# Optimization experiments

Measured on AMD Instinct MI355X. Metric: run time of the kernel, lower is better.

The kernel has to match this reference:

```python
import jax, jax.numpy as jnp
import numpy as np

EPS = 1e-6
NEG_SLOPE = 0.2


def _basis(J):
    # J: [B,N,E,3] -> R: [B,N,E,3(k: U,V,J rows),3(xyz comp)]
    nJ = J / (jnp.linalg.norm(J, axis=-1, keepdims=True) + EPS)
    sub = nJ[..., :2]
    u_z = -(sub[..., 0] ** 2 + sub[..., 1] ** 2) / (nJ[..., 2] + EPS)
    U = jnp.concatenate([sub, u_z[..., None]], axis=-1)
    U = U / (jnp.linalg.norm(U, axis=-1, keepdims=True) + EPS)
    V = jnp.cross(U, nJ)
    return jnp.stack([U, V, nJ], axis=-2)


def _complex_linear(X, J, A, Bw, Cw):
    R = _basis(J)                                   # [B,N,E,3,3], R[...,k,i]
    RtX = jnp.einsum('bneki,bnek->bnei', R, X)      # (R^T X)_i = sum_k R[k,i] X_k
    # rrtx(i, s) has component k equal to R[...,k,i] * s
    a_term = R[..., 0] * RtX[..., 0:1] + R[..., 1] * RtX[..., 1:2]
    b_term = R[..., 1] * RtX[..., 0:1] - R[..., 0] * RtX[..., 1:2]
    c_term = R[..., 2] * RtX[..., 2:3]
    Y = (jnp.einsum('fe,bnei->bnfi', A, a_term)
         + jnp.einsum('fe,bnei->bnfi', Bw, b_term)
         + jnp.einsum('fe,bnei->bnfi', Cw, c_term))
    return Y                                        # [B,N,F,3]


def _vn_leaky_relu(x, W, negative_slope):
    # x: [B,F,3,N]; W: [F,F] torch Linear weight (out,in)
    d = jnp.einsum('gf,bfin->bgin', W, x)
    dot = jnp.sum(x * d, axis=2, keepdims=True)
    d_norm_sq = jnp.sum(d * d, axis=2, keepdims=True)
    neg_branch = x - (dot / (d_norm_sq + EPS)) * d
    lin = jnp.where(dot >= 0, x, neg_branch)
    return negative_slope * x + (1.0 - negative_slope) * lin


def setup_inputs() -> dict:
    key = jax.random.key(0)
    kX, kJ, kA, kB, kC, kW = jax.random.split(key, 6)
    B, N, E, F = 16, 1024, 256, 256
    X = jax.random.normal(kX, (B, N, E, 3), dtype=jnp.float32)
    J = jax.random.normal(kJ, (B, N, E, 3), dtype=jnp.float32)
    A = jax.random.normal(kA, (F, E), dtype=jnp.float32)
    Bw = jax.random.normal(kB, (F, E), dtype=jnp.float32)
    Cw = jax.random.normal(kC, (F, E), dtype=jnp.float32)
    W = jax.random.normal(kW, (F, F), dtype=jnp.float32) * (1.0 / np.sqrt(F))
    return {"X": X, "J": J, "A": A, "Bw": Bw, "Cw": Cw, "W": W, "device": 0}


def reference(X, J, A, Bw, Cw, W, device):
    Y = _complex_linear(X, J, A, Bw, Cw)            # [B,N,F,3]
    x = jnp.transpose(Y, (0, 2, 3, 1))              # [B,F,3,N]
    return _vn_leaky_relu(x, W, NEG_SLOPE)
```

## Files before the change

### kernel.cpp

```cpp
#include <hip/hip_runtime.h>

typedef __attribute__((ext_vector_type(8))) _Float16 half8;
typedef __attribute__((ext_vector_type(4))) _Float16 half4v;
typedef __attribute__((ext_vector_type(4))) float f32x4;
typedef float f32x4u __attribute__((ext_vector_type(4), aligned(4)));
typedef float f32x2u __attribute__((ext_vector_type(2), aligned(4)));

#define EPSF 1e-6f

__device__ __forceinline__ void glds16(const void* g, void* l) {
    __builtin_amdgcn_global_load_lds(
        (const __attribute__((address_space(1))) unsigned*)g,
        (__attribute__((address_space(3))) unsigned*)l, 16, 0, 0);
}
__device__ __forceinline__ unsigned short h2u(_Float16 h) {
    union { _Float16 h; unsigned short u; } c; c.h = h; return c.u;
}

__global__ __launch_bounds__(256) void prep_kernel(
    const float* __restrict__ A, const float* __restrict__ Bw,
    const float* __restrict__ Cw, const float* __restrict__ W,
    _Float16* __restrict__ Mh, _Float16* __restrict__ Wh)
{
    int f = blockIdx.x, e = threadIdx.x;
    Mh[f * 768 + e]       = (_Float16)A[f * 256 + e];
    Mh[f * 768 + 256 + e] = (_Float16)Bw[f * 256 + e];
    Mh[f * 768 + 512 + e] = (_Float16)Cw[f * 256 + e];
    Wh[f * 256 + e]       = (_Float16)W[f * 256 + e];
}

__global__ __launch_bounds__(512, 4) void fused1_kernel(
    const float* __restrict__ X, const float* __restrict__ Jp,
    const _Float16* __restrict__ Mh, _Float16* __restrict__ Y)
{
    extern __shared__ char lds[];
    const int T_OFF = 49152;
    int tid = threadIdx.x;
    int b  = blockIdx.x >> 5;
    int n0 = (blockIdx.x & 31) * 32;

    int l = tid & 63, lr = l & 15, lq = l >> 4;
    int w = tid >> 6, wc = w & 1, wf = w >> 1;
    int nl = tid >> 4, ep = tid & 15;

    size_t pb0 = ((size_t)((b * 1024 + n0 + nl) * 256) + 2 * ep) * 3;

    auto loadXJ = [&](int eb, float* xs, float* js) {
        size_t pb = pb0 + (size_t)eb * 96;
        f32x4u xa = *(const f32x4u*)(X + pb);
        f32x2u xb = *(const f32x2u*)(X + pb + 4);
        f32x4u ja = *(const f32x4u*)(Jp + pb);
        f32x2u jb = *(const f32x2u*)(Jp + pb + 4);
        xs[0]=xa[0]; xs[1]=xa[1]; xs[2]=xa[2]; xs[3]=xa[3]; xs[4]=xb[0]; xs[5]=xb[1];
        js[0]=ja[0]; js[1]=ja[1]; js[2]=ja[2]; js[3]=ja[3]; js[4]=jb[0]; js[5]=jb[1];
    };

    auto stageA = [&](int eb) {
        #pragma unroll
        for (int h = 0; h < 6; ++h) {
            int m = h * 512 + tid;
            int t = m >> 10, fr = (m >> 2) & 255, slot = m & 3;
            size_t go = ((size_t)fr * 768 + t * 256 + eb * 32
                         + ((slot ^ ((fr >> 1) & 3)) * 8)) * 2;
            glds16((const char*)Mh + go, lds + m * 16);
        }
    };

    auto computeT = [&](const float* xs, const float* js) {
        unsigned short hv[2][9];
        #pragma unroll
        for (int p = 0; p < 2; ++p) {
            float x0 = xs[3*p], x1 = xs[3*p+1], x2 = xs[3*p+2];
            float j0 = js[3*p], j1 = js[3*p+1], j2 = js[3*p+2];
            float jj  = j0*j0 + j1*j1 + j2*j2;
            float rn  = __builtin_amdgcn_rcpf(__builtin_amdgcn_sqrtf(jj) + EPSF);
            float nj0 = j0*rn, nj1 = j1*rn, nj2 = j2*rn;
            float s2  = nj0*nj0 + nj1*nj1;
            float uz  = -s2 * __builtin_amdgcn_rcpf(nj2 + EPSF);
            float ru  = __builtin_amdgcn_rcpf(__builtin_amdgcn_sqrtf(s2 + uz*uz) + EPSF);
            float u0 = nj0*ru, u1 = nj1*ru, u2 = uz*ru;
            float v0 = u1*nj2 - u2*nj1;
            float v1 = u2*nj0 - u0*nj2;
            float v2 = u0*nj1 - u1*nj0;
            float r0 = u0*x0 + v0*x1 + nj0*x2;
            float r1 = u1*x0 + v1*x1 + nj1*x2;
            float r2 = u2*x0 + v2*x1 + nj2*x2;
            hv[p][0] = h2u((_Float16)(u0*r0 + u1*r1));
            hv[p][1] = h2u((_Float16)(v0*r0 + v1*r1));
            hv[p][2] = h2u((_Float16)(nj0*r0 + nj1*r1));
            hv[p][3] = h2u((_Float16)(u1*r0 - u0*r1));
            hv[p][4] = h2u((_Float16)(v1*r0 - v0*r1));
            hv[p][5] = h2u((_Float16)(nj1*r0 - nj0*r1));
            hv[p][6] = h2u((_Float16)(u2*r2));
            hv[p][7] = h2u((_Float16)(v2*r2));
            hv[p][8] = h2u((_Float16)(nj2*r2));
        }
        #pragma unroll
        for (int s = 0; s < 9; ++s) {
            int t = s / 3, i = s % 3;
            unsigned pk = (unsigned)hv[0][s] | ((unsigned)hv[1][s] << 16);
            *(unsigned*)(lds + T_OFF + (t * 96 + i * 32 + nl) * 80 + ep * 4) = pk;
        }
    };

    f32x4 acc[3][4] = {};
    float xs[6], js[6];
    loadXJ(0, xs, js);

    for (int eb = 0; eb < 8; ++eb) {
        __syncthreads();
        stageA(eb);
        computeT(xs, js);
        __syncthreads();
        if (eb < 7) loadXJ(eb + 1, xs, js);

        #pragma unroll
        for (int t = 0; t < 3; ++t) {
            half8 af[4], bf[3];
            #pragma unroll
            for (int mi = 0; mi < 4; ++mi) {
                int f = wf * 64 + mi * 16 + lr;
                af[mi] = *(const half8*)(lds + t * 16384 + f * 64
                                         + ((lq ^ ((f >> 1) & 3)) * 16));
            }
            #pragma unroll
            for (int bi = 0; bi < 3; ++bi) {
                int cr = wc * 48 + bi * 16 + lr;
                bf[bi] = *(const half8*)(lds + T_OFF + (t * 96 + cr) * 80 + lq * 16);
            }
            #pragma unroll
            for (int bi = 0; bi < 3; ++bi)
                #pragma unroll
                for (int mi = 0; mi < 4; ++mi)
                    acc[bi][mi] = __builtin_amdgcn_mfma_f32_16x16x32_f16(af[mi], bf[bi], acc[bi][mi], 0, 0, 0);
        }
    }

    #pragma unroll
    for (int bi = 0; bi < 3; ++bi) {
        int cr = wc * 48 + bi * 16 + lr;
        int i = cr >> 5, nl2 = cr & 31;
        size_t rowb = ((size_t)b * 3072 + i * 1024 + n0 + nl2) * 256;
        #pragma unroll
        for (int mi = 0; mi < 4; ++mi) {
            int fb = wf * 64 + mi * 16 + lq * 4;
            f32x4 v = acc[bi][mi];
            half4v p;
            p.x = (_Float16)v[0]; p.y = (_Float16)v[1];
            p.z = (_Float16)v[2]; p.w = (_Float16)v[3];
            *(half4v*)(Y + rowb + fb) = p;
        }
    }
}

__global__ __launch_bounds__(256) void gemm2_kernel(
    const _Float16* __restrict__ Wh, const _Float16* __restrict__ Y,
    float* __restrict__ out, int b_off)
{
    __shared__ char lds[65536];
    int tid = threadIdx.x;
    int bid = blockIdx.x;
    int b   = bid / 64;
    int rt  = bid % 64;
    int g0  = (rt >> 4) * 64;
    int n0  = (rt & 15) * 64;
    size_t bC = (size_t)b * 3072;

    auto stage = [&](int buf, int kt) {
        char* la = lds + buf * 32768;
        char* lb = la + 24576;
        int k0 = kt * 64;
        int wv = (tid >> 6) * 1024;
        #pragma unroll
        for (int h = 0; h < 6; ++h) {
            int m = h * 256 + tid;
            int row = m >> 3, slot = m & 7;
            int cg = (row >> 6) * 1024 + n0 + (row & 63);
            unsigned sw = (slot * 16) ^ ((row & 7) << 4);
            size_t go = ((bC + cg) * 256 + k0) * 2 + sw;
            glds16((const char*)Y + go, la + h * 4096 + wv);
        }
        #pragma unroll
        for (int h = 0; h < 2; ++h) {
            int m = h * 256 + tid;
            int row = m >> 3, slot = m & 7;
            unsigned sw = (slot * 16) ^ ((row & 7) << 4);
            size_t go = ((size_t)(g0 + row) * 256 + k0) * 2 + sw;
            glds16((const char*)Wh + go, lb + h * 4096 + wv);
        }
    };

    int l = tid & 63, lr = l & 15, lq = l >> 4;
    int w = tid >> 6, wn = w & 1, wg = w >> 1;

    f32x4 acc[3][2][2] = {};
    stage(0, 0);
    __syncthreads();

    for (int kt = 0; kt < 4; ++kt) {
        int cur = kt & 1;
        if (kt < 3) stage(cur ^ 1, kt + 1);
        const char* la = lds + cur * 32768;
        const char* lb = la + 24576;
        #pragma unroll
        for (int kk = 0; kk < 2; ++kk) {
            half8 af[3][2], bg[2];
            #pragma unroll
            for (int i = 0; i < 3; ++i)
                #pragma unroll
                for (int nc = 0; nc < 2; ++nc) {
                    int R = i * 64 + wn * 32 + nc * 16 + lr;
                    af[i][nc] = *(const half8*)(la + R * 128 + (((kk * 4 + lq) * 16) ^ ((R & 7) << 4)));
                }
            #pragma unroll
            for (int gf = 0; gf < 2; ++gf) {
                int R = wg * 32 + gf * 16 + lr;
                bg[gf] = *(const half8*)(lb + R * 128 + (((kk * 4 + lq) * 16) ^ ((R & 7) << 4)));
            }
            #pragma unroll
            for (int i = 0; i < 3; ++i)
                #pragma unroll
                for (int nc = 0; nc < 2; ++nc)
                    #pragma unroll
                    for (int gf = 0; gf < 2; ++gf)
                        acc[i][nc][gf] = __builtin_amdgcn_mfma_f32_16x16x32_f16(af[i][nc], bg[gf], acc[i][nc][gf], 0, 0, 0);
        }
        __syncthreads();
    }

    int b_g = b_off + b;
    #pragma unroll
    for (int nc = 0; nc < 2; ++nc)
        #pragma unroll
        for (int gf = 0; gf < 2; ++gf) {
            int g  = g0 + wg * 32 + gf * 16 + lr;
            int nb = n0 + wn * 32 + nc * 16 + lq * 4;
            float x[3][4];
            #pragma unroll
            for (int i = 0; i < 3; ++i)
                #pragma unroll
                for (int r = 0; r < 4; ++r)
                    x[i][r] = (float)Y[(bC + i * 1024 + nb + r) * 256 + g];
            f32x4 o[3];
            #pragma unroll
            for (int r = 0; r < 4; ++r) {
                float d0 = acc[0][nc][gf][r], d1 = acc[1][nc][gf][r], d2 = acc[2][nc][gf][r];
                float dot = x[0][r] * d0 + x[1][r] * d1 + x[2][r] * d2;
                float dn  = d0 * d0 + d1 * d1 + d2 * d2;
                float sc  = dot / (dn + EPSF);
                bool pos  = dot >= 0.0f;
                float l0 = pos ? x[0][r] : fmaf(-sc, d0, x[0][r]);
                float l1 = pos ? x[1][r] : fmaf(-sc, d1, x[1][r]);
                float l2 = pos ? x[2][r] : fmaf(-sc, d2, x[2][r]);
                o[0][r] = fmaf(0.8f, l0, 0.2f * x[0][r]);
                o[1][r] = fmaf(0.8f, l1, 0.2f * x[1][r]);
                o[2][r] = fmaf(0.8f, l2, 0.2f * x[2][r]);
            }
            #pragma unroll
            for (int i = 0; i < 3; ++i)
                *(f32x4*)(out + ((size_t)(b_g * 256 + g) * 3 + i) * 1024 + nb) = o[i];
        }
}

extern "C" void kernel_launch(void* const* d_in, const int* in_sizes, int n_in,
                              void* d_out, int out_size, void* d_ws, size_t ws_size,
                              hipStream_t stream)
{
    const float* X  = (const float*)d_in[0];
    const float* J  = (const float*)d_in[1];
    const float* A  = (const float*)d_in[2];
    const float* Bw = (const float*)d_in[3];
    const float* Cw = (const float*)d_in[4];
    const float* W  = (const float*)d_in[5];
    float* out = (float*)d_out;

    char* ws = (char*)d_ws;
    _Float16* Mh = (_Float16*)ws;
    _Float16* Wh = (_Float16*)(ws + 393216);
    _Float16* Y  = (_Float16*)(ws + 524288);

    hipLaunchKernelGGL(prep_kernel,   dim3(256),  dim3(256), 0, stream,
                       A, Bw, Cw, W, Mh, Wh);
    hipLaunchKernelGGL(fused1_kernel, dim3(512),  dim3(512), 72192, stream,
                       X, J, Mh, Y);
    hipLaunchKernelGGL(gemm2_kernel,  dim3(1024), dim3(256), 0, stream,
                       Wh, Y, out, 0);
}
```

Baseline: 66.89 us.

## Fuse second GEMM and VN leaky ReLU into first kernel via LDS-resident Y

Merges the second GEMM (W times Y) and the vector-neuron leaky ReLU epilogue into the first fused kernel. The fp16 Y tile is written into swizzled LDS instead of global memory, and W fragments are read straight from global into registers with double buffering. This removes the Y round trip through global memory and one kernel launch. In exchange each block must do the whole 256-wide output-feature GEMM for its 32 points, which raises per-block work and register pressure, and W is re-read from global/L2 by every block.

```diff
diff --git a/kernel.cpp b/kernel.cpp
--- a/kernel.cpp
+++ b/kernel.cpp
@@ -29,9 +29,10 @@
     Wh[f * 256 + e]       = (_Float16)W[f * 256 + e];
 }
 
-__global__ __launch_bounds__(512, 4) void fused1_kernel(
+__global__ __launch_bounds__(512, 4) void fused_kernel(
     const float* __restrict__ X, const float* __restrict__ Jp,
-    const _Float16* __restrict__ Mh, _Float16* __restrict__ Y)
+    const _Float16* __restrict__ Mh, const _Float16* __restrict__ Wh,
+    float* __restrict__ out)
 {
     extern __shared__ char lds[];
     const int T_OFF = 49152;
@@ -136,130 +137,86 @@
         }
     }
 
+    __syncthreads();
     #pragma unroll
     for (int bi = 0; bi < 3; ++bi) {
-        int cr = wc * 48 + bi * 16 + lr;
-        int i = cr >> 5, nl2 = cr & 31;
-        size_t rowb = ((size_t)b * 3072 + i * 1024 + n0 + nl2) * 256;
+        int c = wc * 48 + bi * 16 + lr;
         #pragma unroll
         for (int mi = 0; mi < 4; ++mi) {
-            int fb = wf * 64 + mi * 16 + lq * 4;
+            int fb2 = (wf * 64 + mi * 16 + lq * 4) * 2;
             f32x4 v = acc[bi][mi];
             half4v p;
             p.x = (_Float16)v[0]; p.y = (_Float16)v[1];
             p.z = (_Float16)v[2]; p.w = (_Float16)v[3];
-            *(half4v*)(Y + rowb + fb) = p;
-        }
-    }
-}
-
-__global__ __launch_bounds__(256) void gemm2_kernel(
-    const _Float16* __restrict__ Wh, const _Float16* __restrict__ Y,
-    float* __restrict__ out, int b_off)
-{
-    __shared__ char lds[65536];
-    int tid = threadIdx.x;
-    int bid = blockIdx.x;
-    int b   = bid / 64;
-    int rt  = bid % 64;
-    int g0  = (rt >> 4) * 64;
-    int n0  = (rt & 15) * 64;
-    size_t bC = (size_t)b * 3072;
-
-    auto stage = [&](int buf, int kt) {
-        char* la = lds + buf * 32768;
-        char* lb = la + 24576;
-        int k0 = kt * 64;
-        int wv = (tid >> 6) * 1024;
-        #pragma unroll
-        for (int h = 0; h < 6; ++h) {
-            int m = h * 256 + tid;
-            int row = m >> 3, slot = m & 7;
-            int cg = (row >> 6) * 1024 + n0 + (row & 63);
-            unsigned sw = (slot * 16) ^ ((row & 7) << 4);
-            size_t go = ((bC + cg) * 256 + k0) * 2 + sw;
-            glds16((const char*)Y + go, la + h * 4096 + wv);
-        }
-        #pragma unroll
-        for (int h = 0; h < 2; ++h) {
-            int m = h * 256 + tid;
-            int row = m >> 3, slot = m & 7;
-            unsigned sw = (slot * 16) ^ ((row & 7) << 4);
-            size_t go = ((size_t)(g0 + row) * 256 + k0) * 2 + sw;
-            glds16((const char*)Wh + go, lb + h * 4096 + wv);
-        }
-    };
-
-    int l = tid & 63, lr = l & 15, lq = l >> 4;
-    int w = tid >> 6, wn = w & 1, wg = w >> 1;
-
-    f32x4 acc[3][2][2] = {};
-    stage(0, 0);
+            *(half4v*)(lds + c * 512 + (fb2 ^ ((c & 7) << 4))) = p;
+        }
+    }
+
+    int nh = w & 1, gw = w >> 1;
+    half8 wreg[2][4];
+    #pragma unroll
+    for (int gf = 0; gf < 4; ++gf) {
+        int g = gw * 64 + gf * 16 + lr;
+        wreg[0][gf] = *(const half8*)(Wh + (size_t)g * 256 + lq * 8);
+    }
     __syncthreads();
 
-    for (int kt = 0; kt < 4; ++kt) {
-        int cur = kt & 1;
-        if (kt < 3) stage(cur ^ 1, kt + 1);
-        const char* la = lds + cur * 32768;
-        const char* lb = la + 24576;
-        #pragma unroll
-        for (int kk = 0; kk < 2; ++kk) {
-            half8 af[3][2], bg[2];
-            #pragma unroll
-            for (int i = 0; i < 3; ++i)
-                #pragma unroll
-                for (int nc = 0; nc < 2; ++nc) {
-                    int R = i * 64 + wn * 32 + nc * 16 + lr;
-                    af[i][nc] = *(const half8*)(la + R * 128 + (((kk * 4 + lq) * 16) ^ ((R & 7) << 4)));
-                }
-            #pragma unroll
-            for (int gf = 0; gf < 2; ++gf) {
-                int R = wg * 32 + gf * 16 + lr;
-                bg[gf] = *(const half8*)(lb + R * 128 + (((kk * 4 + lq) * 16) ^ ((R & 7) << 4)));
-            }
-            #pragma unroll
-            for (int i = 0; i < 3; ++i)
-                #pragma unroll
-                for (int nc = 0; nc < 2; ++nc)
-                    #pragma unroll
-                    for (int gf = 0; gf < 2; ++gf)
-                        acc[i][nc][gf] = __builtin_amdgcn_mfma_f32_16x16x32_f16(af[i][nc], bg[gf], acc[i][nc][gf], 0, 0, 0);
-        }
-        __syncthreads();
-    }
-
-    int b_g = b_off + b;
-    #pragma unroll
-    for (int nc = 0; nc < 2; ++nc)
-        #pragma unroll
-        for (int gf = 0; gf < 2; ++gf) {
-            int g  = g0 + wg * 32 + gf * 16 + lr;
-            int nb = n0 + wn * 32 + nc * 16 + lq * 4;
-            float x[3][4];
-            #pragma unroll
-            for (int i = 0; i < 3; ++i)
-                #pragma unroll
-                for (int r = 0; r < 4; ++r)
-                    x[i][r] = (float)Y[(bC + i * 1024 + nb + r) * 256 + g];
-            f32x4 o[3];
-            #pragma unroll
-            for (int r = 0; r < 4; ++r) {
-                float d0 = acc[0][nc][gf][r], d1 = acc[1][nc][gf][r], d2 = acc[2][nc][gf][r];
-                float dot = x[0][r] * d0 + x[1][r] * d1 + x[2][r] * d2;
-                float dn  = d0 * d0 + d1 * d1 + d2 * d2;
-                float sc  = dot / (dn + EPSF);
-                bool pos  = dot >= 0.0f;
-                float l0 = pos ? x[0][r] : fmaf(-sc, d0, x[0][r]);
-                float l1 = pos ? x[1][r] : fmaf(-sc, d1, x[1][r]);
-                float l2 = pos ? x[2][r] : fmaf(-sc, d2, x[2][r]);
-                o[0][r] = fmaf(0.8f, l0, 0.2f * x[0][r]);
-                o[1][r] = fmaf(0.8f, l1, 0.2f * x[1][r]);
-                o[2][r] = fmaf(0.8f, l2, 0.2f * x[2][r]);
-            }
-            #pragma unroll
-            for (int i = 0; i < 3; ++i)
-                *(f32x4*)(out + ((size_t)(b_g * 256 + g) * 3 + i) * 1024 + nb) = o[i];
-        }
+    f32x4 acc2[3][4] = {};
+    #pragma unroll
+    for (int kt = 0; kt < 8; ++kt) {
+        if (kt < 7) {
+            #pragma unroll
+            for (int gf = 0; gf < 4; ++gf) {
+                int g = gw * 64 + gf * 16 + lr;
+                wreg[(kt + 1) & 1][gf] =
+                    *(const half8*)(Wh + (size_t)g * 256 + (kt + 1) * 32 + lq * 8);
+            }
+        }
+        half8 yf[3];
+        #pragma unroll
+        for (int ci = 0; ci < 3; ++ci) {
+            int c = ci * 32 + nh * 16 + lr;
+            yf[ci] = *(const half8*)(lds + c * 512
+                                     + ((kt * 64 + lq * 16) ^ ((c & 7) << 4)));
+        }
+        #pragma unroll
+        for (int ci = 0; ci < 3; ++ci)
+            #pragma unroll
+            for (int gf = 0; gf < 4; ++gf)
+                acc2[ci][gf] = __builtin_amdgcn_mfma_f32_16x16x32_f16(
+                    yf[ci], wreg[kt & 1][gf], acc2[ci][gf], 0, 0, 0);
+    }
+
+    #pragma unroll
+    for (int gf = 0; gf < 4; ++gf) {
+        int g = gw * 64 + gf * 16 + lr;
+        f32x4 o[3];
+        #pragma unroll
+        for (int r = 0; r < 4; ++r) {
+            float xv[3];
+            #pragma unroll
+            for (int ci = 0; ci < 3; ++ci) {
+                int c = ci * 32 + nh * 16 + lq * 4 + r;
+                xv[ci] = (float)*(const _Float16*)(lds + c * 512
+                                 + ((g * 2) ^ ((c & 7) << 4)));
+            }
+            float d0 = acc2[0][gf][r], d1 = acc2[1][gf][r], d2 = acc2[2][gf][r];
+            float dot = xv[0] * d0 + xv[1] * d1 + xv[2] * d2;
+            float dn  = d0 * d0 + d1 * d1 + d2 * d2;
+            float sc  = dot / (dn + EPSF);
+            bool pos  = dot >= 0.0f;
+            float l0 = pos ? xv[0] : fmaf(-sc, d0, xv[0]);
+            float l1 = pos ? xv[1] : fmaf(-sc, d1, xv[1]);
+            float l2 = pos ? xv[2] : fmaf(-sc, d2, xv[2]);
+            o[0][r] = fmaf(0.8f, l0, 0.2f * xv[0]);
+            o[1][r] = fmaf(0.8f, l1, 0.2f * xv[1]);
+            o[2][r] = fmaf(0.8f, l2, 0.2f * xv[2]);
+        }
+        int nb = n0 + nh * 16 + lq * 4;
+        #pragma unroll
+        for (int i = 0; i < 3; ++i)
+            *(f32x4*)(out + ((size_t)(b * 256 + g) * 3 + i) * 1024 + nb) = o[i];
+    }
 }
 
 extern "C" void kernel_launch(void* const* d_in, const int* in_sizes, int n_in,
@@ -277,12 +234,12 @@
     char* ws = (char*)d_ws;
     _Float16* Mh = (_Float16*)ws;
     _Float16* Wh = (_Float16*)(ws + 393216);
-    _Float16* Y  = (_Float16*)(ws + 524288);
-
-    hipLaunchKernelGGL(prep_kernel,   dim3(256),  dim3(256), 0, stream,
+
+    (void)hipFuncSetAttribute((const void*)fused_kernel,
+                              hipFuncAttributeMaxDynamicSharedMemorySize, 72192);
+
+    hipLaunchKernelGGL(prep_kernel,  dim3(256), dim3(256), 0, stream,
                        A, Bw, Cw, W, Mh, Wh);
-    hipLaunchKernelGGL(fused1_kernel, dim3(512),  dim3(512), 72192, stream,
-                       X, J, Mh, Y);
-    hipLaunchKernelGGL(gemm2_kernel,  dim3(1024), dim3(256), 0, stream,
-                       Wh, Y, out, 0);
-}
+    hipLaunchKernelGGL(fused_kernel, dim3(512), dim3(512), 72192, stream,
+                       X, J, Mh, Wh, out);
+}
```

Result: faster. 58.56 us (-12.5%).
